# Kernel optimization log

Hardware: AMD Instinct MI355X
Metric: run time of the kernel (lower is better)

The kernel has to match this reference:

```python
import jax, jax.numpy as jnp
import numpy as np
import math

B, W, D, H, K = 32, 512, 512, 8, 64
DH = D // H

def _rms(x, s, eps=1e-6):
    return x / jnp.sqrt(jnp.mean(x * x, axis=-1, keepdims=True) + eps) * s

def _l2n(x):
    return x / (jnp.linalg.norm(x, axis=-1, keepdims=True) + 1e-6)

def _rope(x, fc):
    b, t, h, d = x.shape
    xc = jax.lax.complex(x[..., 0::2], x[..., 1::2])
    xr = xc * fc
    return jnp.stack([xr.real, xr.imag], axis=-1).reshape(b, t, h, d)

def setup_inputs() -> dict:
    key = jax.random.key(0)
    ks = jax.random.split(key, 24)
    n = lambda i, s: jax.random.normal(ks[i], s, jnp.float32) * 0.02
    return {
        'x': jax.random.normal(ks[0], (B, W, D), jnp.float32),
        'epi_keys': _l2n(jax.random.normal(ks[1], (B, K, D), jnp.float32)),
        'epi_vals': jax.random.normal(ks[2], (B, K, D), jnp.float32),
        'epi_age': jax.random.uniform(ks[3], (B, K), jnp.float32, 0.0, 10.0),
        'epi_strength': jax.random.uniform(ks[4], (B, K), jnp.float32, 0.01, 1.0),
        'pos_idx': jnp.arange(W, dtype=jnp.int32),
        'rms1': jnp.ones((D,), jnp.float32), 'rms_kv': jnp.ones((D,), jnp.float32),
        'rms2': jnp.ones((D,), jnp.float32), 'rms_read': jnp.ones((D,), jnp.float32),
        'Wq': n(5, (D, D)), 'bq': jnp.zeros((D,), jnp.float32),
        'Wk': n(6, (D, D)), 'bk': jnp.zeros((D,), jnp.float32),
        'Wv': n(7, (D, D)), 'bv': jnp.zeros((D,), jnp.float32),
        'Wo': n(8, (D, D)), 'bo': jnp.zeros((D,), jnp.float32),
        'W1': n(9, (D, 8 * D)), 'W2': n(10, (4 * D, D)),
        'Wwk': n(11, (D, D)), 'bwk': jnp.zeros((D,), jnp.float32),
        'Wwv': n(12, (D, D)), 'bwv': jnp.zeros((D,), jnp.float32),
        'Wws': n(13, (D, 1)), 'bws': jnp.zeros((1,), jnp.float32),
        'Wg1': n(14, (D + 2, D)), 'bg1': jnp.zeros((D,), jnp.float32),
        'Wg2': n(15, (D, 1)), 'bg2': jnp.zeros((1,), jnp.float32),
    }

def _cell(x, epi_keys, epi_vals, epi_age, epi_strength, pos_idx,
          rms1, rms_kv, rms2, rms_read, Wq, bq, Wk, bk, Wv, bv, Wo, bo,
          W1, W2, Wwk, bwk, Wwv, bwv, Wws, bws, Wg1, bg1, Wg2, bg2):
    Bc, T, Dc = x.shape
    # RoPE freqs at absolute window positions (slice_freqs_cis)
    freqs = 1.0 / (10000.0 ** (jnp.arange(0, DH, 2, dtype=jnp.float32) / DH))  # (DH/2,)
    ang = pos_idx.astype(jnp.float32)[:, None] * freqs[None, :]               # (T, DH/2)
    fc = jax.lax.complex(jnp.cos(ang), jnp.sin(ang))[None, :, None, :]        # (1,T,1,DH/2)
    # --- windowed causal RoPE attention (TransformerBlock) ---
    nx, nkv = _rms(x, rms1), _rms(x, rms_kv)
    q = _rope((nx @ Wq + bq).reshape(Bc, T, H, DH), fc)
    k = _rope((nkv @ Wk + bk).reshape(Bc, T, H, DH), fc)
    v = (nkv @ Wv + bv).reshape(Bc, T, H, DH)
    att = jnp.einsum('bthd,bshd->bhts', q, k) / math.sqrt(DH)
    causal = jnp.tril(jnp.ones((T, T), bool))
    att = jnp.where(causal[None, None], att, -1e9)
    p = jax.nn.softmax(att, axis=-1)
    o = jnp.einsum('bhts,bshd->bthd', p, v).reshape(Bc, T, Dc)
    h1 = x + (o @ Wo + bo)
    gv = _rms(h1, rms2) @ W1
    g, val = jnp.split(gv, 2, axis=-1)
    h2 = h1 + (jax.nn.silu(g) * val) @ W2                                     # (B,T,D)
    # --- window summary query ---
    q_win = jnp.mean(h2, axis=1)                                              # (B,D)
    # --- EpisodicSlotReader ---
    qn = _l2n(q_win)
    kn = _l2n(epi_keys)
    sim_r = jnp.sum(kn * qn[:, None, :], axis=-1)                             # (B,K)
    logits = sim_r + 0.5 * jnp.log(jnp.clip(epi_strength, 0.001, 1e9)) - 0.02 * epi_age
    logits = logits + ((epi_strength > 0.001).astype(jnp.float32) - 1.0) * 1000.0
    w_read = jax.nn.softmax(logits, axis=-1)
    read = _rms(jnp.sum(w_read[:, :, None] * epi_vals, axis=1), rms_read)     # (B,D)
    # --- write projections ---
    write_key = q_win @ Wwk + bwk
    write_val = q_win @ Wwv + bwv
    ws = jnp.clip(jax.nn.sigmoid(q_win @ Wws + bws), 0.0, 1.0)                # (B,1)
    # --- EpisodicSlotWriter (ST top-1 competitive write) ---
    wk_n = _l2n(write_key)
    sim_w = jnp.sum(kn * wk_n[:, None, :], axis=-1)                           # (B,K)
    soft = jax.nn.softmax(sim_w * 50.0, axis=-1)
    hard = jax.nn.one_hot(jnp.argmax(soft, axis=-1), K, dtype=jnp.float32)
    write_w = jax.lax.stop_gradient(hard - soft) + soft
    eff = write_w * ws * 0.5                                                  # (B,K)
    re = eff[:, :, None]
    keys_new = _l2n((1.0 - re) * epi_keys + re * write_key[:, None, :])
    vals_new = (1.0 - re) * epi_vals + re * write_val[:, None, :]
    age_new = (epi_age + 1.0) * (1.0 - write_w)
    sn = epi_strength * 0.995
    sn = jnp.clip(sn + write_w * ws * (1.0 - sn), 0.001, 1.0)
    best_sim = jnp.max(sim_w, axis=-1)                                        # (B,)
    # --- MemoryRecallGate ---
    novelty = (1.0 - best_sim)[:, None]
    xg = jnp.concatenate([q_win, ws, novelty], axis=-1)                       # (B,D+2)
    gate = jax.nn.sigmoid(jax.nn.silu(xg @ Wg1 + bg1) @ Wg2 + bg2)            # (B,1)
    out = h2 + (gate * read)[:, None, :]
    return out, keys_new, vals_new, age_new, sn, gate

def reference(x, epi_keys, epi_vals, epi_age, epi_strength, pos_idx,
              rms1, rms_kv, rms2, rms_read, Wq, bq, Wk, bk, Wv, bv, Wo, bo,
              W1, W2, Wwk, bwk, Wwv, bwv, Wws, bws, Wg1, bg1, Wg2, bg2):
    return _cell(x, epi_keys, epi_vals, epi_age, epi_strength, pos_idx,
                 rms1, rms_kv, rms2, rms_read, Wq, bq, Wk, bk, Wv, bv, Wo, bo,
                 W1, W2, Wwk, bwk, Wwv, bwv, Wws, bws, Wg1, bg1, Wg2, bg2)
```

## Files before the change

### kernel.cpp

```cpp
#include <hip/hip_runtime.h>


#define DEVI __device__ __forceinline__
typedef unsigned short u16;
typedef unsigned int   u32;
typedef __bf16 v8bf __attribute__((ext_vector_type(8)));
typedef float  v4f  __attribute__((ext_vector_type(4)));

DEVI float bf2f(u16 u) { u32 v = ((u32)u) << 16; return __builtin_bit_cast(float, v); }
DEVI u16 f2bf(float f) {
  u32 x = __builtin_bit_cast(u32, f);
  u32 r = x + 0x7fffu + ((x >> 16) & 1u);
  return (u16)(r >> 16);
}
DEVI uint4 pack8(const float* f) {
  u32 a[4];
#pragma unroll
  for (int i = 0; i < 4; ++i)
    a[i] = (u32)f2bf(f[2*i]) | ((u32)f2bf(f[2*i+1]) << 16);
  uint4 v; v.x = a[0]; v.y = a[1]; v.z = a[2]; v.w = a[3]; return v;
}
DEVI void ld8f(const float* p, float* f) {
  float4 a = *(const float4*)p, b = *(const float4*)(p + 4);
  f[0]=a.x; f[1]=a.y; f[2]=a.z; f[3]=a.w; f[4]=b.x; f[5]=b.y; f[6]=b.z; f[7]=b.w;
}
DEVI void st8f(float* p, const float* f) {
  *(float4*)p       = make_float4(f[0], f[1], f[2], f[3]);
  *(float4*)(p + 4) = make_float4(f[4], f[5], f[6], f[7]);
}
DEVI v8bf ldfrag(const u16* p) { return __builtin_bit_cast(v8bf, *(const uint4*)p); }

DEVI u32 rot1(u32 w, float c, float s) {
  float e = bf2f((u16)(w & 0xffffu)), o = bf2f((u16)(w >> 16));
  float ne = e * c - o * s;
  float no = e * s + o * c;
  return (u32)f2bf(ne) | ((u32)f2bf(no) << 16);
}

DEVI void async16(const u16* g, u16* l) {
  __builtin_amdgcn_global_load_lds(
      (const __attribute__((address_space(1))) void*)g,
      (__attribute__((address_space(3))) void*)l, 16, 0, 0);
}

DEVI float wave_sum64(float v) {
  v += __shfl_xor(v, 1);  v += __shfl_xor(v, 2);  v += __shfl_xor(v, 4);
  v += __shfl_xor(v, 8);  v += __shfl_xor(v, 16); v += __shfl_xor(v, 32);
  return v;
}

__device__ float block_sum256(float v, float* sred) {
  v = wave_sum64(v);
  int w = threadIdx.x >> 6;
  __syncthreads();
  if ((threadIdx.x & 63) == 0) sred[w] = v;
  __syncthreads();
  return sred[0] + sred[1] + sred[2] + sred[3];
}

__global__ __launch_bounds__(256) void prep_k(
    const float* __restrict__ Wq, const float* __restrict__ Wk,
    const float* __restrict__ Wv, const float* __restrict__ Wo,
    const float* __restrict__ W1, const float* __restrict__ W2,
    const float* __restrict__ rms1, const float* __restrict__ rms_kv,
    const float* __restrict__ rms2, u16* __restrict__ WTqkv,
    u16* __restrict__ WTo, u16* __restrict__ WT1, u16* __restrict__ WT2,
    const float* __restrict__ bq, const float* __restrict__ bk,
    const float* __restrict__ bv, float* __restrict__ bias_qkv,
    const int* __restrict__ pos, float* __restrict__ tbl,
    float* __restrict__ qw_g, const float* __restrict__ x,
    u16* __restrict__ nrm) {
  int id = blockIdx.x;
  int tid = threadIdx.x;
  if (id >= 4230) {
    int w = tid >> 6, lane = tid & 63;
    size_t row = (size_t)(id - 4230) * 4 + w;
    float xf[8]; ld8f(x + row * 512 + lane * 8, xf);
    float ss = 0.f;
#pragma unroll
    for (int i = 0; i < 8; ++i) ss += xf[i] * xf[i];
    ss = wave_sum64(ss);
    float inv = rsqrtf(ss * (1.f / 512.f) + 1e-6f);
    float of[8];
#pragma unroll
    for (int i = 0; i < 8; ++i) of[i] = xf[i] * inv;
    *(uint4*)(nrm + row * 512 + lane * 8) = pack8(of);
    return;
  }
  if (id >= 4166) {
    qw_g[(id - 4166) * 256 + tid] = 0.f;
    return;
  }
  if (id >= 4102) {
    int idx = (id - 4102) * 256 + tid;
    int t = idx >> 5, f = idx & 31;
    float freq = exp2f(-0.41524101186f * (float)f);
    float ang = (float)pos[t] * freq;
    float sv, cv;
    sincosf(ang, &sv, &cv);
    tbl[t * 64 + f * 2]     = cv;
    tbl[t * 64 + f * 2 + 1] = sv;
    return;
  }
  if (id >= 4096) {
    int j = (id - 4096) * 256 + tid;
    bias_qkv[j] = j < 512 ? bq[j] : (j < 1024 ? bk[j - 512] : bv[j - 1024]);
    return;
  }
  const float* in; const float* scale; u16* outp; int R, C, bx, by;
  if (id < 256)       { in=Wq; scale=rms1;   outp=WTqkv;            R=512;  C=512;  int l=id;       bx=l&15;  by=l>>4; }
  else if (id < 512)  { in=Wk; scale=rms_kv; outp=WTqkv+512*512;    R=512;  C=512;  int l=id-256;   bx=l&15;  by=l>>4; }
  else if (id < 768)  { in=Wv; scale=rms_kv; outp=WTqkv+1024*512;   R=512;  C=512;  int l=id-512;   bx=l&15;  by=l>>4; }
  else if (id < 1024) { in=Wo; scale=nullptr;outp=WTo;              R=512;  C=512;  int l=id-768;   bx=l&15;  by=l>>4; }
  else if (id < 3072) { in=W1; scale=rms2;   outp=WT1;              R=512;  C=4096; int l=id-1024;  bx=l&127; by=l>>7; }
  else                { in=W2; scale=nullptr;outp=WT2;              R=2048; C=512;  int l=id-3072;  bx=l&15;  by=l>>4; }
  __shared__ u16 t[32][33];
  int c0 = bx * 32, r0 = by * 32;
  int lc = tid & 31, lr = tid >> 5;
  for (int rr = lr; rr < 32; rr += 8) {
    float v = in[(size_t)(r0 + rr) * C + c0 + lc];
    if (scale) v *= scale[r0 + rr];
    t[rr][lc] = f2bf(v);
  }
  __syncthreads();
  for (int rr = lr; rr < 32; rr += 8)
    outp[(size_t)(c0 + rr) * R + r0 + lc] = t[lc][rr];
}

__global__ __launch_bounds__(256) void rms_k(const float* __restrict__ x,
                                             u16* __restrict__ o1) {
  int w = threadIdx.x >> 6, lane = threadIdx.x & 63;
  size_t row = (size_t)blockIdx.x * 4 + w;
  float xf[8]; ld8f(x + row * 512 + lane * 8, xf);
  float ss = 0.f;
#pragma unroll
  for (int i = 0; i < 8; ++i) ss += xf[i] * xf[i];
  ss = wave_sum64(ss);
  float inv = rsqrtf(ss * (1.f / 512.f) + 1e-6f);
  float of[8];
#pragma unroll
  for (int i = 0; i < 8; ++i) of[i] = xf[i] * inv;
  *(uint4*)(o1 + row * 512 + lane * 8) = pack8(of);
}

__global__ __launch_bounds__(256) void gemm128_k(const u16* __restrict__ A,
                                                 const u16* __restrict__ BT,
                                                 const float* __restrict__ bias,
                                                 const float* __restrict__ resf,
                                                 u16* __restrict__ outb,
                                                 float* __restrict__ outf,
                                                 int N, int Kd) {
  __shared__ u16 As[128 * 64];
  __shared__ u16 Bs[128 * 64];
  int tid = threadIdx.x;
  int w = tid >> 6, lane = tid & 63;
  int m = lane & 15, quad = lane >> 4;
  int wm = w >> 1, wn = w & 1;
  int bm = blockIdx.x, bn = blockIdx.y;
  v4f acc[4][4] = {};
  const int gswz = ((lane & 7) ^ (lane >> 3)) * 8;
  const u16* Ag = A + (size_t)(bm * 128 + w * 32 + (lane >> 3)) * Kd + gswz;
  const u16* Bg = BT + (size_t)(bn * 128 + w * 32 + (lane >> 3)) * Kd + gswz;
  u16* Al = &As[w * 32 * 64];
  u16* Bl = &Bs[w * 32 * 64];
  const int rsw = (m & 7) * 8;
  for (int k0 = 0; k0 < Kd; k0 += 64) {
#pragma unroll
    for (int it = 0; it < 4; ++it) {
      async16(Ag + (size_t)it * 8 * Kd + k0, Al + it * 8 * 64);
      async16(Bg + (size_t)it * 8 * Kd + k0, Bl + it * 8 * 64);
    }
    __syncthreads();
#pragma unroll
    for (int kk = 0; kk < 2; ++kk) {
      v8bf af[4], bfr[4];
#pragma unroll
      for (int i = 0; i < 4; ++i)
        af[i] = ldfrag(&As[(wm * 64 + i * 16 + m) * 64 +
                           ((kk * 32 + quad * 8) ^ rsw)]);
#pragma unroll
      for (int j = 0; j < 4; ++j)
        bfr[j] = ldfrag(&Bs[(wn * 64 + j * 16 + m) * 64 +
                            ((kk * 32 + quad * 8) ^ rsw)]);
#pragma unroll
      for (int i = 0; i < 4; ++i)
#pragma unroll
        for (int j = 0; j < 4; ++j)
          acc[i][j] = __builtin_amdgcn_mfma_f32_16x16x32_bf16(af[i], bfr[j],
                                                              acc[i][j], 0, 0, 0);
    }
    __syncthreads();
  }
#pragma unroll
  for (int i = 0; i < 4; ++i) {
    int grow0 = bm * 128 + wm * 64 + i * 16 + quad * 4;
#pragma unroll
    for (int j = 0; j < 4; ++j) {
      int gcol = bn * 128 + wn * 64 + j * 16 + m;
      float bv = bias ? bias[gcol] : 0.f;
#pragma unroll
      for (int rr = 0; rr < 4; ++rr) {
        size_t idx = (size_t)(grow0 + rr) * N + gcol;
        float v = acc[i][j][rr] + bv;
        if (resf) v += resf[idx];
        if (outb) outb[idx] = f2bf(v);
        else      outf[idx] = v;
      }
    }
  }
}

__global__ __launch_bounds__(256) void mlp1_k(const u16* __restrict__ A,
                                              const u16* __restrict__ W1T,
                                              u16* __restrict__ out) {
  __shared__ u16 As[128 * 64];
  __shared__ u16 Bgs[64 * 64];
  __shared__ u16 Bvs[64 * 64];
  const int Kd = 512;
  int tid = threadIdx.x;
  int w = tid >> 6, lane = tid & 63;
  int m = lane & 15, quad = lane >> 4;
  int bm = blockIdx.x, bn = blockIdx.y;
  v4f accg[2][4] = {}, accv[2][4] = {};
  const int gswz = ((lane & 7) ^ (lane >> 3)) * 8;
  const u16* Ag  = A + (size_t)(bm * 128 + w * 32 + (lane >> 3)) * Kd + gswz;
  const u16* Bgp = W1T + (size_t)(bn * 64 + w * 16 + (lane >> 3)) * Kd + gswz;
  const u16* Bvp = W1T + (size_t)(2048 + bn * 64 + w * 16 + (lane >> 3)) * Kd + gswz;
  u16* Al  = &As[w * 32 * 64];
  u16* Bgl = &Bgs[w * 16 * 64];
  u16* Bvl = &Bvs[w * 16 * 64];
  const int rsw = (m & 7) * 8;
  for (int k0 = 0; k0 < Kd; k0 += 64) {
#pragma unroll
    for (int it = 0; it < 4; ++it)
      async16(Ag + (size_t)it * 8 * Kd + k0, Al + it * 8 * 64);
#pragma unroll
    for (int it = 0; it < 2; ++it) {
      async16(Bgp + (size_t)it * 8 * Kd + k0, Bgl + it * 8 * 64);
      async16(Bvp + (size_t)it * 8 * Kd + k0, Bvl + it * 8 * 64);
    }
    __syncthreads();
#pragma unroll
    for (int kk = 0; kk < 2; ++kk) {
      v8bf af[2], bg[4], bv[4];
#pragma unroll
      for (int i = 0; i < 2; ++i)
        af[i] = ldfrag(&As[(w * 32 + i * 16 + m) * 64 +
                           ((kk * 32 + quad * 8) ^ rsw)]);
#pragma unroll
      for (int j = 0; j < 4; ++j) {
        bg[j] = ldfrag(&Bgs[(j * 16 + m) * 64 + ((kk * 32 + quad * 8) ^ rsw)]);
        bv[j] = ldfrag(&Bvs[(j * 16 + m) * 64 + ((kk * 32 + quad * 8) ^ rsw)]);
      }
#pragma unroll
      for (int i = 0; i < 2; ++i)
#pragma unroll
        for (int j = 0; j < 4; ++j) {
          accg[i][j] = __builtin_amdgcn_mfma_f32_16x16x32_bf16(af[i], bg[j],
                                                               accg[i][j], 0, 0, 0);
          accv[i][j] = __builtin_amdgcn_mfma_f32_16x16x32_bf16(af[i], bv[j],
                                                               accv[i][j], 0, 0, 0);
        }
    }
    __syncthreads();
  }
#pragma unroll
  for (int i = 0; i < 2; ++i) {
    int grow0 = bm * 128 + w * 32 + i * 16 + quad * 4;
#pragma unroll
    for (int j = 0; j < 4; ++j) {
      int gcol = bn * 64 + j * 16 + m;
#pragma unroll
      for (int rr = 0; rr < 4; ++rr) {
        float g = accg[i][j][rr];
        float sv = g / (1.f + __expf(-g));
        out[(size_t)(grow0 + rr) * 2048 + gcol] = f2bf(sv * accv[i][j][rr]);
      }
    }
  }
}

__global__ __launch_bounds__(1024) void attn_k(const u16* __restrict__ qkv,
                                               const float* __restrict__ tbl,
                                               u16* __restrict__ og) {
  __shared__ u16 Ks[512 * 64];
  __shared__ u16 Vt[64 * 512];
  __shared__ u16 Ps[16][16 * 40];
  int tid = threadIdx.x;
  int w = tid >> 6, lane = tid & 63;
  int m = lane & 15, quad = lane >> 4;
  int bh = blockIdx.x;
  int b = bh >> 3, h = bh & 7;
  const size_t qbase = (size_t)b * 512 * 1536 + h * 64;
  const size_t obase = (size_t)b * 512 * 512 + h * 64;
  const u16* kbase = qkv + (size_t)b * 512 * 1536 + 512 + h * 64;
  const u16* vbase = kbase + 512;

  {
    int d8 = (tid & 7) * 8;
    for (int s = tid >> 3; s < 512; s += 128) {
      uint4 t4 = *(const uint4*)(kbase + (size_t)s * 1536 + d8);
      const float4* tp = (const float4*)(tbl + s * 64 + d8);
      float4 cs01 = tp[0], cs23 = tp[1];
      t4.x = rot1(t4.x, cs01.x, cs01.y);
      t4.y = rot1(t4.y, cs01.z, cs01.w);
      t4.z = rot1(t4.z, cs23.x, cs23.y);
      t4.w = rot1(t4.w, cs23.z, cs23.w);
      *(uint4*)&Ks[s * 64 + (d8 ^ ((s & 7) * 8))] = t4;
    }
  }
  {
    int d = tid & 63, sw = (d & 7) * 8;
    for (int s = tid >> 6; s < 512; s += 16)
      Vt[d * 512 + (s ^ sw)] = vbase[(size_t)s * 1536 + d];
  }
  __syncthreads();

  for (int rep = 0; rep < 2; ++rep) {
    int qt = rep == 0 ? w : 31 - w;
    int tb = qt * 16;
    const u16* qp = qkv + qbase + (size_t)(tb + m) * 1536;
    uint4 q0 = *(const uint4*)(qp + quad * 8);
    uint4 q1 = *(const uint4*)(qp + 32 + quad * 8);
    {
      const float* tq = tbl + (tb + m) * 64;
      float4 a = *(const float4*)(tq + quad * 8);
      float4 b4 = *(const float4*)(tq + quad * 8 + 4);
      q0.x = rot1(q0.x, a.x, a.y);   q0.y = rot1(q0.y, a.z, a.w);
      q0.z = rot1(q0.z, b4.x, b4.y); q0.w = rot1(q0.w, b4.z, b4.w);
      float4 c4 = *(const float4*)(tq + 32 + quad * 8);
      float4 d4 = *(const float4*)(tq + 36 + quad * 8);
      q1.x = rot1(q1.x, c4.x, c4.y); q1.y = rot1(q1.y, c4.z, c4.w);
      q1.z = rot1(q1.z, d4.x, d4.y); q1.w = rot1(q1.w, d4.z, d4.w);
    }
    v8bf aq0 = __builtin_bit_cast(v8bf, q0);
    v8bf aq1 = __builtin_bit_cast(v8bf, q1);
    v4f acc[4] = {};
    float mr[4], lr_[4];
#pragma unroll
    for (int rr = 0; rr < 4; ++rr) { mr[rr] = -1.0e30f; lr_[rr] = 0.f; }
    int swz = (m & 7) * 8;

    for (int st2 = 0; st2 <= qt; st2 += 2) {
      int srA = st2 * 16 + m;
      v8bf ka0 = ldfrag(&Ks[srA * 64 + ((quad * 8) ^ swz)]);
      v8bf ka1 = ldfrag(&Ks[srA * 64 + ((32 + quad * 8) ^ swz)]);
      v4f s4a = {};
      __builtin_amdgcn_s_setprio(1);
      s4a = __builtin_amdgcn_mfma_f32_16x16x32_bf16(aq0, ka0, s4a, 0, 0, 0);
      s4a = __builtin_amdgcn_mfma_f32_16x16x32_bf16(aq1, ka1, s4a, 0, 0, 0);
      __builtin_amdgcn_s_setprio(0);
      bool haveB = (st2 + 1 <= qt);
      v4f s4b = {};
      if (haveB) {
        int srB = srA + 16;
        v8bf kb0 = ldfrag(&Ks[srB * 64 + ((quad * 8) ^ swz)]);
        v8bf kb1 = ldfrag(&Ks[srB * 64 + ((32 + quad * 8) ^ swz)]);
        __builtin_amdgcn_s_setprio(1);
        s4b = __builtin_amdgcn_mfma_f32_16x16x32_bf16(aq0, kb0, s4b, 0, 0, 0);
        s4b = __builtin_amdgcn_mfma_f32_16x16x32_bf16(aq1, kb1, s4b, 0, 0, 0);
        __builtin_amdgcn_s_setprio(0);
      }
      float sca[4], scb[4];
#pragma unroll
      for (int rr = 0; rr < 4; ++rr) {
        int rowt = tb + quad * 4 + rr;
        sca[rr] = s4a[rr] * 0.125f;
        if (st2 == qt && st2 * 16 + m > rowt) sca[rr] = -1.0e9f;
        scb[rr] = haveB ? s4b[rr] * 0.125f : -1.0e30f;
        if (haveB && st2 + 1 == qt && (st2 + 1) * 16 + m > rowt) scb[rr] = -1.0e9f;
      }
      float pva[4], pvb[4], alpha[4];
#pragma unroll
      for (int rr = 0; rr < 4; ++rr) {
        float v = fmaxf(sca[rr], scb[rr]);
        v = fmaxf(v, __shfl_xor(v, 1));
        v = fmaxf(v, __shfl_xor(v, 2));
        v = fmaxf(v, __shfl_xor(v, 4));
        v = fmaxf(v, __shfl_xor(v, 8));
        float mn = fmaxf(mr[rr], v);
        alpha[rr] = __expf(mr[rr] - mn);
        pva[rr] = __expf(sca[rr] - mn);
        pvb[rr] = __expf(scb[rr] - mn);
        mr[rr] = mn;
      }
#pragma unroll
      for (int rr = 0; rr < 4; ++rr) {
        float s = pva[rr] + pvb[rr];
        s += __shfl_xor(s, 1); s += __shfl_xor(s, 2);
        s += __shfl_xor(s, 4); s += __shfl_xor(s, 8);
        lr_[rr] = lr_[rr] * alpha[rr] + s;
#pragma unroll
        for (int c = 0; c < 4; ++c) acc[c][rr] *= alpha[rr];
        Ps[w][(quad * 4 + rr) * 40 + m]      = f2bf(pva[rr]);
        Ps[w][(quad * 4 + rr) * 40 + 16 + m] = f2bf(pvb[rr]);
      }
      __asm__ volatile("" ::: "memory");
      v8bf pf = ldfrag(&Ps[w][m * 40 + quad * 8]);
      __builtin_amdgcn_s_setprio(1);
#pragma unroll
      for (int c = 0; c < 4; ++c) {
        int drow = c * 16 + m;
        v8bf vf = ldfrag(&Vt[drow * 512 +
                             ((st2 * 16 + quad * 8) ^ ((drow & 7) * 8))]);
        acc[c] = __builtin_amdgcn_mfma_f32_16x16x32_bf16(pf, vf, acc[c], 0, 0, 0);
      }
      __builtin_amdgcn_s_setprio(0);
    }
#pragma unroll
    for (int rr = 0; rr < 4; ++rr) {
      int t = tb + quad * 4 + rr;
      float inv = 1.f / lr_[rr];
      u16* op = og + obase + (size_t)t * 512;
#pragma unroll
      for (int c = 0; c < 4; ++c) op[c * 16 + m] = f2bf(acc[c][rr] * inv);
    }
  }
}

__global__ __launch_bounds__(256) void qwsum_k(const float* __restrict__ h2,
                                               float* __restrict__ qw_g) {
  int bc = blockIdx.x;
  int b = bc >> 3;
  int c = bc & 7;
  int d2 = threadIdx.x * 2;
  float a0 = 0.f, a1 = 0.f;
  for (int i = 0; i < 64; ++i) {
    int t = c * 64 + i;
    float2 v = *(const float2*)(h2 + ((size_t)(b * 512 + t)) * 512 + d2);
    a0 += v.x;
    a1 += v.y;
  }
  atomicAdd(qw_g + (size_t)b * 512 + d2,     a0 * (1.f / 512.f));
  atomicAdd(qw_g + (size_t)b * 512 + d2 + 1, a1 * (1.f / 512.f));
}

__global__ __launch_bounds__(256) void gemv_k(
    const float* __restrict__ qw_g, const float* __restrict__ Wwk,
    const float* __restrict__ bwk, const float* __restrict__ Wwv,
    const float* __restrict__ bwv, const float* __restrict__ Wg1,
    const float* __restrict__ bg1, const float* __restrict__ Wws,
    const float* __restrict__ bws, float* __restrict__ wkey_g,
    float* __restrict__ wval_g, float* __restrict__ abase_g,
    float* __restrict__ ws_g) {
  __shared__ float qs[512];
  __shared__ float prt[4][64];
  __shared__ float sred[8];
  int tid = threadIdx.x;
  int b = blockIdx.y, cg = blockIdx.x;
  qs[tid]       = qw_g[(size_t)b * 512 + tid];
  qs[tid + 256] = qw_g[(size_t)b * 512 + tid + 256];
  __syncthreads();
  if (cg == 24) {
    float p = qs[tid] * Wws[tid] + qs[tid + 256] * Wws[tid + 256];
    float tot = block_sum256(p, sred);
    if (tid == 0) {
      float wsv = 1.f / (1.f + __expf(-(tot + bws[0])));
      ws_g[b] = fminf(fmaxf(wsv, 0.f), 1.f);
    }
    return;
  }
  int sel = cg >> 3;
  int c0 = (cg & 7) * 64;
  const float* W = sel == 0 ? Wwk : (sel == 1 ? Wwv : Wg1);
  const float* bias = sel == 0 ? bwk : (sel == 1 ? bwv : bg1);
  float* dst = sel == 0 ? wkey_g : (sel == 1 ? wval_g : abase_g);
  int kg = tid >> 6, cl = tid & 63;
  const float* Wp = W + (size_t)(kg * 128) * 512 + c0 + cl;
  float acc = 0.f;
#pragma unroll 8
  for (int i = 0; i < 128; ++i) acc += qs[kg * 128 + i] * Wp[(size_t)i * 512];
  prt[kg][cl] = acc;
  __syncthreads();
  if (tid < 64)
    dst[(size_t)b * 512 + c0 + tid] =
        prt[0][tid] + prt[1][tid] + prt[2][tid] + prt[3][tid] + bias[c0 + tid];
}

__global__ __launch_bounds__(256) void epi2_k(
    const float* __restrict__ qw_g, const float* __restrict__ wkey_g,
    const float* __restrict__ wval_g, const float* __restrict__ abase_g,
    const float* __restrict__ ws_g, const float* __restrict__ keys,
    const float* __restrict__ vals, const float* __restrict__ age,
    const float* __restrict__ strength, const float* __restrict__ Wg1,
    const float* __restrict__ Wg2, const float* __restrict__ bg2,
    const float* __restrict__ rms_read, float* __restrict__ read_f,
    float* __restrict__ gate_f, float* __restrict__ keys_out,
    float* __restrict__ vals_out, float* __restrict__ age_out,
    float* __restrict__ sn_out, float* __restrict__ gate_out) {
  int b = blockIdx.x;
  int tid = threadIdx.x;
  int w = tid >> 6, lane = tid & 63;
  __shared__ float qs[512], wkl[512], wvl[512];
  __shared__ float knorm[64], sr[64], swv[64], wread[64];
  __shared__ float sred[8];
  __shared__ float scal[2];
  __shared__ int bestk;
  __shared__ float novs;

  qs[tid]        = qw_g[(size_t)b * 512 + tid];
  qs[tid + 256]  = qw_g[(size_t)b * 512 + tid + 256];
  wkl[tid]       = wkey_g[(size_t)b * 512 + tid];
  wkl[tid + 256] = wkey_g[(size_t)b * 512 + tid + 256];
  wvl[tid]       = wval_g[(size_t)b * 512 + tid];
  wvl[tid + 256] = wval_g[(size_t)b * 512 + tid + 256];
  __syncthreads();
  float ws_s = ws_g[b];
  float p = qs[tid] * qs[tid] + qs[tid + 256] * qs[tid + 256];
  float tot = block_sum256(p, sred);
  if (tid == 0) scal[0] = 1.f / (sqrtf(tot) + 1e-6f);
  p = wkl[tid] * wkl[tid] + wkl[tid + 256] * wkl[tid + 256];
  tot = block_sum256(p, sred);
  if (tid == 0) scal[1] = 1.f / (sqrtf(tot) + 1e-6f);
  __syncthreads();
  float qscale = scal[0], wscale = scal[1];
  for (int k = w; k < 64; k += 4) {
    float kf[8];
    ld8f(keys + ((size_t)b * 64 + k) * 512 + lane * 8, kf);
    float s2 = 0.f, sq = 0.f, sw = 0.f;
#pragma unroll
    for (int i = 0; i < 8; ++i) {
      s2 += kf[i] * kf[i];
      sq += kf[i] * qs[lane * 8 + i];
      sw += kf[i] * wkl[lane * 8 + i];
    }
    s2 = wave_sum64(s2);
    sq = wave_sum64(sq);
    sw = wave_sum64(sw);
    if (lane == 0) {
      float kn = sqrtf(s2) + 1e-6f;
      knorm[k] = kn;
      float st = strength[b * 64 + k];
      float ag = age[b * 64 + k];
      sr[k] = (sq * qscale) / kn + 0.5f * logf(fminf(fmaxf(st, 0.001f), 1e9f)) -
              0.02f * ag + ((st > 0.001f) ? 0.f : -1000.f);
      swv[k] = (sw * wscale) / kn;
    }
  }
  __syncthreads();
  if (w == 0) {
    float v = sr[lane];
    float mx = v;
    mx = fmaxf(mx, __shfl_xor(mx, 1));  mx = fmaxf(mx, __shfl_xor(mx, 2));
    mx = fmaxf(mx, __shfl_xor(mx, 4));  mx = fmaxf(mx, __shfl_xor(mx, 8));
    mx = fmaxf(mx, __shfl_xor(mx, 16)); mx = fmaxf(mx, __shfl_xor(mx, 32));
    float e = __expf(v - mx);
    float sm = wave_sum64(e);
    wread[lane] = e / sm;
  } else if (w == 1) {
    float v = swv[lane];
    int idx = lane;
#pragma unroll
    for (int mm = 1; mm < 64; mm <<= 1) {
      float ov = __shfl_xor(v, mm);
      int oi = __shfl_xor(idx, mm);
      if (ov > v || (ov == v && oi < idx)) { v = ov; idx = oi; }
    }
    if (lane == 0) { bestk = idx; novs = 1.f - v; }
  }
  __syncthreads();
  float rv0 = 0.f, rv1 = 0.f;
  for (int k = 0; k < 64; ++k) {
    float wr = wread[k];
    const float* vp = vals + ((size_t)b * 64 + k) * 512;
    rv0 += wr * vp[tid];
    rv1 += wr * vp[tid + 256];
  }
  p = rv0 * rv0 + rv1 * rv1;
  tot = block_sum256(p, sred);
  float rinv = rsqrtf(tot * (1.f / 512.f) + 1e-6f);
  read_f[(size_t)b * 512 + tid]       = rv0 * rinv * rms_read[tid];
  read_f[(size_t)b * 512 + tid + 256] = rv1 * rinv * rms_read[tid + 256];
  if (tid < 64) {
    int k = tid;
    float hard = (k == bestk) ? 1.f : 0.f;
    float ag = age[b * 64 + k];
    age_out[b * 64 + k] = (ag + 1.f) * (1.f - hard);
    float st = strength[b * 64 + k];
    float s0 = st * 0.995f;
    float snv = s0 + hard * ws_s * (1.f - s0);
    sn_out[b * 64 + k] = fminf(fmaxf(snv, 0.001f), 1.f);
  }
  for (int k = w; k < 64; k += 4) {
    float re = (k == bestk) ? ws_s * 0.5f : 0.f;
    float kf[8], vf[8];
    ld8f(keys + ((size_t)b * 64 + k) * 512 + lane * 8, kf);
    ld8f(vals + ((size_t)b * 64 + k) * 512 + lane * 8, vf);
    float u[8], ss = 0.f;
#pragma unroll
    for (int i = 0; i < 8; ++i) {
      u[i] = (1.f - re) * kf[i] + re * wkl[lane * 8 + i];
      ss += u[i] * u[i];
    }
    ss = wave_sum64(ss);
    float uinv = 1.f / (sqrtf(ss) + 1e-6f);
    float ko[8], vo[8];
#pragma unroll
    for (int i = 0; i < 8; ++i) {
      ko[i] = u[i] * uinv;
      vo[i] = (1.f - re) * vf[i] + re * wvl[lane * 8 + i];
    }
    st8f(keys_out + ((size_t)b * 64 + k) * 512 + lane * 8, ko);
    st8f(vals_out + ((size_t)b * 64 + k) * 512 + lane * 8, vo);
  }
  __syncthreads();
  float nov = novs;
  float a0 = abase_g[(size_t)b * 512 + tid] +
             ws_s * Wg1[(size_t)512 * 512 + tid] +
             nov * Wg1[(size_t)513 * 512 + tid];
  float a1 = abase_g[(size_t)b * 512 + tid + 256] +
             ws_s * Wg1[(size_t)512 * 512 + tid + 256] +
             nov * Wg1[(size_t)513 * 512 + tid + 256];
  float h0 = a0 / (1.f + __expf(-a0));
  float h1v = a1 / (1.f + __expf(-a1));
  float gp = h0 * Wg2[tid] + h1v * Wg2[tid + 256];
  tot = block_sum256(gp, sred);
  if (tid == 0) {
    float g = 1.f / (1.f + __expf(-(tot + bg2[0])));
    gate_f[b] = g;
    gate_out[b] = g;
  }
}

__global__ __launch_bounds__(256) void final_k(const float* __restrict__ h2,
                                               const float* __restrict__ read_f,
                                               const float* __restrict__ gate_f,
                                               float* __restrict__ outp) {
  size_t i2 = ((size_t)blockIdx.x * 256 + threadIdx.x) * 2;
  int b = (int)(i2 >> 18);
  int d = (int)(i2 & 511);
  float g = gate_f[b];
  float2 h = *(const float2*)(h2 + i2);
  outp[i2]     = h.x + g * read_f[b * 512 + d];
  outp[i2 + 1] = h.y + g * read_f[b * 512 + d + 1];
}

extern "C" void kernel_launch(void* const* d_in, const int* in_sizes, int n_in,
                              void* d_out, int out_size, void* d_ws,
                              size_t ws_size, hipStream_t stream) {
  const float* x        = (const float*)d_in[0];
  const float* epi_keys = (const float*)d_in[1];
  const float* epi_vals = (const float*)d_in[2];
  const float* epi_age  = (const float*)d_in[3];
  const float* epi_str  = (const float*)d_in[4];
  const int*   pos      = (const int*)d_in[5];
  const float* rms1     = (const float*)d_in[6];
  const float* rms_kv   = (const float*)d_in[7];
  const float* rms2     = (const float*)d_in[8];
  const float* rms_read = (const float*)d_in[9];
  const float* Wq = (const float*)d_in[10]; const float* bq = (const float*)d_in[11];
  const float* Wk = (const float*)d_in[12]; const float* bk = (const float*)d_in[13];
  const float* Wv = (const float*)d_in[14]; const float* bv = (const float*)d_in[15];
  const float* Wo = (const float*)d_in[16]; const float* bo = (const float*)d_in[17];
  const float* W1 = (const float*)d_in[18]; const float* W2 = (const float*)d_in[19];
  const float* Wwk = (const float*)d_in[20]; const float* bwk = (const float*)d_in[21];
  const float* Wwv = (const float*)d_in[22]; const float* bwv = (const float*)d_in[23];
  const float* Wws = (const float*)d_in[24]; const float* bws = (const float*)d_in[25];
  const float* Wg1 = (const float*)d_in[26]; const float* bg1 = (const float*)d_in[27];
  const float* Wg2 = (const float*)d_in[28]; const float* bg2 = (const float*)d_in[29];

  float* out      = (float*)d_out;
  float* out_main = out;
  float* out_keys = out + 8388608;
  float* out_vals = out + 9437184;
  float* out_age  = out + 10485760;
  float* out_sn   = out + 10487808;
  float* out_gate = out + 10489856;

  char* w8 = (char*)d_ws;
  size_t off = 0;
  auto alloc = [&](size_t bytes) {
    char* pp = w8 + off;
    off += (bytes + 255) & ~(size_t)255;
    return pp;
  };
  u16* WTqkv = (u16*)alloc((size_t)1536 * 512 * 2);
  u16* WTo   = (u16*)alloc(512 * 512 * 2);
  u16* WT1   = (u16*)alloc((size_t)4096 * 512 * 2);
  u16* WT2   = (u16*)alloc((size_t)512 * 2048 * 2);
  const size_t TB = (size_t)16384 * 512 * 2;
  u16* nrm  = (u16*)alloc(TB);
  u16* qkvb = (u16*)alloc(3 * TB);
  u16* ob   = (u16*)alloc(TB);
  u16* n2   = (u16*)alloc(TB);
  float* h1f = (float*)alloc((size_t)16384 * 512 * 4);
  u16*   gact = nrm;
  float* h2f  = (float*)ob;
  float* bias_qkv = (float*)alloc(1536 * 4);
  float* tbl      = (float*)alloc((size_t)512 * 64 * 4);
  float* qw_g    = (float*)alloc((size_t)32 * 512 * 4);
  float* wkey_g  = (float*)alloc((size_t)32 * 512 * 4);
  float* wval_g  = (float*)alloc((size_t)32 * 512 * 4);
  float* abase_g = (float*)alloc((size_t)32 * 512 * 4);
  float* ws_g    = (float*)alloc(64 * 4);
  float* read_f  = (float*)alloc((size_t)32 * 512 * 4);
  float* gate_f  = (float*)alloc(64 * 4);

  prep_k<<<8326, 256, 0, stream>>>(Wq, Wk, Wv, Wo, W1, W2, rms1, rms_kv, rms2,
                                   WTqkv, WTo, WT1, WT2, bq, bk, bv, bias_qkv,
                                   pos, tbl, qw_g, x, nrm);
  gemm128_k<<<dim3(128, 12), 256, 0, stream>>>(nrm, WTqkv, bias_qkv, nullptr,
                                               qkvb, nullptr, 1536, 512);
  attn_k<<<256, 1024, 0, stream>>>(qkvb, tbl, ob);
  gemm128_k<<<dim3(128, 4), 256, 0, stream>>>(ob, WTo, bo, x,
                                              nullptr, h1f, 512, 512);
  rms_k<<<4096, 256, 0, stream>>>(h1f, n2);
  mlp1_k<<<dim3(128, 32), 256, 0, stream>>>(n2, WT1, gact);
  gemm128_k<<<dim3(128, 4), 256, 0, stream>>>(gact, WT2, nullptr, h1f,
                                              nullptr, h2f, 512, 2048);
  qwsum_k<<<256, 256, 0, stream>>>(h2f, qw_g);
  gemv_k<<<dim3(25, 32), 256, 0, stream>>>(qw_g, Wwk, bwk, Wwv, bwv, Wg1, bg1,
                                           Wws, bws, wkey_g, wval_g, abase_g, ws_g);
  epi2_k<<<32, 256, 0, stream>>>(qw_g, wkey_g, wval_g, abase_g, ws_g, epi_keys,
                                 epi_vals, epi_age, epi_str, Wg1, Wg2, bg2,
                                 rms_read, read_f, gate_f, out_keys, out_vals,
                                 out_age, out_sn, out_gate);
  final_k<<<16384, 256, 0, stream>>>(h2f, read_f, gate_f, out_main);
}
```

Baseline: 497.2 us.

## Fuse window-mean into W2 GEMM epilogue, fold gemv into epi kernel, vectorize V load

```diff
diff --git a/kernel.cpp b/kernel.cpp
--- a/kernel.cpp
+++ b/kernel.cpp
@@ -149,6 +149,7 @@
                                                  const float* __restrict__ resf,
                                                  u16* __restrict__ outb,
                                                  float* __restrict__ outf,
+                                                 float* __restrict__ colsum,
                                                  int N, int Kd) {
   __shared__ u16 As[128 * 64];
   __shared__ u16 Bs[128 * 64];
@@ -191,6 +192,7 @@
     }
     __syncthreads();
   }
+  float csum[4] = {0.f, 0.f, 0.f, 0.f};
 #pragma unroll
   for (int i = 0; i < 4; ++i) {
     int grow0 = bm * 128 + wm * 64 + i * 16 + quad * 4;
@@ -205,7 +207,23 @@
         if (resf) v += resf[idx];
         if (outb) outb[idx] = f2bf(v);
         else      outf[idx] = v;
-      }
+        if (colsum) csum[j] += v;
+      }
+    }
+  }
+  if (colsum) {
+    float* cs = (float*)As;
+    __syncthreads();
+    if (tid < 128) cs[tid] = 0.f;
+    __syncthreads();
+    int lc = wn * 64 + m;
+#pragma unroll
+    for (int j = 0; j < 4; ++j) atomicAdd(&cs[lc + j * 16], csum[j]);
+    __syncthreads();
+    if (tid < 128) {
+      int b = bm >> 2;
+      atomicAdd(colsum + (size_t)b * 512 + bn * 128 + tid,
+                cs[tid] * (1.f / 512.f));
     }
   }
 }
@@ -310,9 +328,16 @@
     }
   }
   {
-    int d = tid & 63, sw = (d & 7) * 8;
-    for (int s = tid >> 6; s < 512; s += 16)
-      Vt[d * 512 + (s ^ sw)] = vbase[(size_t)s * 1536 + d];
+    int d0 = (tid & 7) * 8;
+    for (int s = tid >> 3; s < 512; s += 128) {
+      uint4 v4 = *(const uint4*)(vbase + (size_t)s * 1536 + d0);
+      const u16* vv = (const u16*)&v4;
+#pragma unroll
+      for (int j = 0; j < 8; ++j) {
+        int d = d0 + j;
+        Vt[d * 512 + (s ^ ((d & 7) * 8))] = vv[j];
+      }
+    }
   }
   __syncthreads();
 
@@ -418,96 +443,52 @@
   }
 }
 
-__global__ __launch_bounds__(256) void qwsum_k(const float* __restrict__ h2,
-                                               float* __restrict__ qw_g) {
-  int bc = blockIdx.x;
-  int b = bc >> 3;
-  int c = bc & 7;
-  int d2 = threadIdx.x * 2;
-  float a0 = 0.f, a1 = 0.f;
-  for (int i = 0; i < 64; ++i) {
-    int t = c * 64 + i;
-    float2 v = *(const float2*)(h2 + ((size_t)(b * 512 + t)) * 512 + d2);
-    a0 += v.x;
-    a1 += v.y;
-  }
-  atomicAdd(qw_g + (size_t)b * 512 + d2,     a0 * (1.f / 512.f));
-  atomicAdd(qw_g + (size_t)b * 512 + d2 + 1, a1 * (1.f / 512.f));
-}
-
-__global__ __launch_bounds__(256) void gemv_k(
-    const float* __restrict__ qw_g, const float* __restrict__ Wwk,
+__global__ __launch_bounds__(256) void epi2_k(
+    const float* __restrict__ qw_g, const float* __restrict__ keys,
+    const float* __restrict__ vals, const float* __restrict__ age,
+    const float* __restrict__ strength, const float* __restrict__ Wwk,
     const float* __restrict__ bwk, const float* __restrict__ Wwv,
     const float* __restrict__ bwv, const float* __restrict__ Wg1,
     const float* __restrict__ bg1, const float* __restrict__ Wws,
-    const float* __restrict__ bws, float* __restrict__ wkey_g,
-    float* __restrict__ wval_g, float* __restrict__ abase_g,
-    float* __restrict__ ws_g) {
-  __shared__ float qs[512];
-  __shared__ float prt[4][64];
-  __shared__ float sred[8];
-  int tid = threadIdx.x;
-  int b = blockIdx.y, cg = blockIdx.x;
-  qs[tid]       = qw_g[(size_t)b * 512 + tid];
-  qs[tid + 256] = qw_g[(size_t)b * 512 + tid + 256];
-  __syncthreads();
-  if (cg == 24) {
-    float p = qs[tid] * Wws[tid] + qs[tid + 256] * Wws[tid + 256];
-    float tot = block_sum256(p, sred);
-    if (tid == 0) {
-      float wsv = 1.f / (1.f + __expf(-(tot + bws[0])));
-      ws_g[b] = fminf(fmaxf(wsv, 0.f), 1.f);
-    }
-    return;
-  }
-  int sel = cg >> 3;
-  int c0 = (cg & 7) * 64;
-  const float* W = sel == 0 ? Wwk : (sel == 1 ? Wwv : Wg1);
-  const float* bias = sel == 0 ? bwk : (sel == 1 ? bwv : bg1);
-  float* dst = sel == 0 ? wkey_g : (sel == 1 ? wval_g : abase_g);
-  int kg = tid >> 6, cl = tid & 63;
-  const float* Wp = W + (size_t)(kg * 128) * 512 + c0 + cl;
-  float acc = 0.f;
-#pragma unroll 8
-  for (int i = 0; i < 128; ++i) acc += qs[kg * 128 + i] * Wp[(size_t)i * 512];
-  prt[kg][cl] = acc;
-  __syncthreads();
-  if (tid < 64)
-    dst[(size_t)b * 512 + c0 + tid] =
-        prt[0][tid] + prt[1][tid] + prt[2][tid] + prt[3][tid] + bias[c0 + tid];
-}
-
-__global__ __launch_bounds__(256) void epi2_k(
-    const float* __restrict__ qw_g, const float* __restrict__ wkey_g,
-    const float* __restrict__ wval_g, const float* __restrict__ abase_g,
-    const float* __restrict__ ws_g, const float* __restrict__ keys,
-    const float* __restrict__ vals, const float* __restrict__ age,
-    const float* __restrict__ strength, const float* __restrict__ Wg1,
-    const float* __restrict__ Wg2, const float* __restrict__ bg2,
-    const float* __restrict__ rms_read, float* __restrict__ read_f,
-    float* __restrict__ gate_f, float* __restrict__ keys_out,
-    float* __restrict__ vals_out, float* __restrict__ age_out,
-    float* __restrict__ sn_out, float* __restrict__ gate_out) {
+    const float* __restrict__ bws, const float* __restrict__ Wg2,
+    const float* __restrict__ bg2, const float* __restrict__ rms_read,
+    float* __restrict__ read_f, float* __restrict__ gate_f,
+    float* __restrict__ keys_out, float* __restrict__ vals_out,
+    float* __restrict__ age_out, float* __restrict__ sn_out,
+    float* __restrict__ gate_out) {
   int b = blockIdx.x;
   int tid = threadIdx.x;
   int w = tid >> 6, lane = tid & 63;
-  __shared__ float qs[512], wkl[512], wvl[512];
+  __shared__ float qs[512], wkl[512], wvl[512], abl[512];
   __shared__ float knorm[64], sr[64], swv[64], wread[64];
   __shared__ float sred[8];
   __shared__ float scal[2];
   __shared__ int bestk;
   __shared__ float novs;
 
-  qs[tid]        = qw_g[(size_t)b * 512 + tid];
-  qs[tid + 256]  = qw_g[(size_t)b * 512 + tid + 256];
-  wkl[tid]       = wkey_g[(size_t)b * 512 + tid];
-  wkl[tid + 256] = wkey_g[(size_t)b * 512 + tid + 256];
-  wvl[tid]       = wval_g[(size_t)b * 512 + tid];
-  wvl[tid + 256] = wval_g[(size_t)b * 512 + tid + 256];
-  __syncthreads();
-  float ws_s = ws_g[b];
-  float p = qs[tid] * qs[tid] + qs[tid + 256] * qs[tid + 256];
+  qs[tid]       = qw_g[(size_t)b * 512 + tid];
+  qs[tid + 256] = qw_g[(size_t)b * 512 + tid + 256];
+  __syncthreads();
+  float p = qs[tid] * Wws[tid] + qs[tid + 256] * Wws[tid + 256];
   float tot = block_sum256(p, sred);
+  float ws_s = 1.f / (1.f + __expf(-(tot + bws[0])));
+  ws_s = fminf(fmaxf(ws_s, 0.f), 1.f);
+#pragma unroll
+  for (int u = 0; u < 2; ++u) {
+    int c = tid + u * 256;
+    float aK = bwk[c], aV = bwv[c], aA = bg1[c];
+#pragma unroll 8
+    for (int i = 0; i < 512; ++i) {
+      float q = qs[i];
+      aK += q * Wwk[(size_t)i * 512 + c];
+      aV += q * Wwv[(size_t)i * 512 + c];
+      aA += q * Wg1[(size_t)i * 512 + c];
+    }
+    wkl[c] = aK; wvl[c] = aV; abl[c] = aA;
+  }
+  __syncthreads();
+  p = qs[tid] * qs[tid] + qs[tid + 256] * qs[tid + 256];
+  tot = block_sum256(p, sred);
   if (tid == 0) scal[0] = 1.f / (sqrtf(tot) + 1e-6f);
   p = wkl[tid] * wkl[tid] + wkl[tid + 256] * wkl[tid + 256];
   tot = block_sum256(p, sred);
@@ -605,10 +586,10 @@
   }
   __syncthreads();
   float nov = novs;
-  float a0 = abase_g[(size_t)b * 512 + tid] +
+  float a0 = abl[tid] +
              ws_s * Wg1[(size_t)512 * 512 + tid] +
              nov * Wg1[(size_t)513 * 512 + tid];
-  float a1 = abase_g[(size_t)b * 512 + tid + 256] +
+  float a1 = abl[tid + 256] +
              ws_s * Wg1[(size_t)512 * 512 + tid + 256] +
              nov * Wg1[(size_t)513 * 512 + tid + 256];
   float h0 = a0 / (1.f + __expf(-a0));
@@ -688,32 +669,25 @@
   float* h2f  = (float*)ob;
   float* bias_qkv = (float*)alloc(1536 * 4);
   float* tbl      = (float*)alloc((size_t)512 * 64 * 4);
-  float* qw_g    = (float*)alloc((size_t)32 * 512 * 4);
-  float* wkey_g  = (float*)alloc((size_t)32 * 512 * 4);
-  float* wval_g  = (float*)alloc((size_t)32 * 512 * 4);
-  float* abase_g = (float*)alloc((size_t)32 * 512 * 4);
-  float* ws_g    = (float*)alloc(64 * 4);
-  float* read_f  = (float*)alloc((size_t)32 * 512 * 4);
-  float* gate_f  = (float*)alloc(64 * 4);
+  float* qw_g     = (float*)alloc((size_t)32 * 512 * 4);
+  float* read_f   = (float*)alloc((size_t)32 * 512 * 4);
+  float* gate_f   = (float*)alloc(64 * 4);
 
   prep_k<<<8326, 256, 0, stream>>>(Wq, Wk, Wv, Wo, W1, W2, rms1, rms_kv, rms2,
                                    WTqkv, WTo, WT1, WT2, bq, bk, bv, bias_qkv,
                                    pos, tbl, qw_g, x, nrm);
   gemm128_k<<<dim3(128, 12), 256, 0, stream>>>(nrm, WTqkv, bias_qkv, nullptr,
-                                               qkvb, nullptr, 1536, 512);
+                                               qkvb, nullptr, nullptr, 1536, 512);
   attn_k<<<256, 1024, 0, stream>>>(qkvb, tbl, ob);
   gemm128_k<<<dim3(128, 4), 256, 0, stream>>>(ob, WTo, bo, x,
-                                              nullptr, h1f, 512, 512);
+                                              nullptr, h1f, nullptr, 512, 512);
   rms_k<<<4096, 256, 0, stream>>>(h1f, n2);
   mlp1_k<<<dim3(128, 32), 256, 0, stream>>>(n2, WT1, gact);
   gemm128_k<<<dim3(128, 4), 256, 0, stream>>>(gact, WT2, nullptr, h1f,
-                                              nullptr, h2f, 512, 2048);
-  qwsum_k<<<256, 256, 0, stream>>>(h2f, qw_g);
-  gemv_k<<<dim3(25, 32), 256, 0, stream>>>(qw_g, Wwk, bwk, Wwv, bwv, Wg1, bg1,
-                                           Wws, bws, wkey_g, wval_g, abase_g, ws_g);
-  epi2_k<<<32, 256, 0, stream>>>(qw_g, wkey_g, wval_g, abase_g, ws_g, epi_keys,
-                                 epi_vals, epi_age, epi_str, Wg1, Wg2, bg2,
-                                 rms_read, read_f, gate_f, out_keys, out_vals,
-                                 out_age, out_sn, out_gate);
+                                              nullptr, h2f, qw_g, 512, 2048);
+  epi2_k<<<32, 256, 0, stream>>>(qw_g, epi_keys, epi_vals, epi_age, epi_str,
+                                 Wwk, bwk, Wwv, bwv, Wg1, bg1, Wws, bws,
+                                 Wg2, bg2, rms_read, read_f, gate_f, out_keys,
+                                 out_vals, out_age, out_sn, out_gate);
   final_k<<<16384, 256, 0, stream>>>(h2f, read_f, gate_f, out_main);
 }
```

Result: slower. 563.6 us (+13.3%).
